# Kernel tuning notes

Measured on AMD Instinct MI355X. Metric: run time of the kernel, lower is better.

The kernel has to match this reference:

```python
import jax, jax.numpy as jnp
import numpy as np

D_IN = 1024
D_OUT = 1024
B = 4
S = 2048


def setup_inputs() -> dict:
    key = jax.random.key(0)
    kx, kq, kk, kv = jax.random.split(key, 4)
    x = jax.random.normal(kx, (B, S, D_IN), dtype=jnp.float32)
    # Linear weights stored as [d_in, d_out] so projection is x @ W
    sc = 1.0 / np.sqrt(D_IN)
    Wq = jax.random.normal(kq, (D_IN, D_OUT), dtype=jnp.float32) * sc
    Wk = jax.random.normal(kk, (D_IN, D_OUT), dtype=jnp.float32) * sc
    Wv = jax.random.normal(kv, (D_IN, D_OUT), dtype=jnp.float32) * sc
    return {"x": x, "Wq": Wq, "Wk": Wk, "Wv": Wv}


def reference(x, Wq, Wk, Wv):
    # q, k, v: [b, s, d_out]
    q = jnp.einsum("bsd,de->bse", x, Wq)
    k = jnp.einsum("bsd,de->bse", x, Wk)
    v = jnp.einsum("bsd,de->bse", x, Wv)
    s = q.shape[1]
    # raw scores [b, s, s]
    scores = jnp.einsum("bqd,bkd->bqk", q, k)
    # causal mask: disallow key j > query i (see notes re: original mask bug)
    causal = jnp.triu(jnp.ones((s, s), dtype=bool), k=1)
    scores = jnp.where(causal[None, :, :], -jnp.inf, scores)
    scale = 1.0 / jnp.sqrt(jnp.asarray(k.shape[-1], dtype=scores.dtype))
    att_weights = jax.nn.softmax(scores * scale, axis=-1)
    # dropout p=0.0 -> identity
    att_output = jnp.einsum("bqk,bkd->bqd", att_weights, v)
    return att_output, att_weights
```

## Files before the change

### kernel.cpp

```cpp
#include <hip/hip_runtime.h>
#include <stdint.h>

#define DIM 1024
#define SEQ 2048
#define NB 4

typedef unsigned short u16;
typedef __bf16 bf16x8 __attribute__((ext_vector_type(8)));
typedef float floatx4 __attribute__((ext_vector_type(4)));

__device__ __forceinline__ u16 f32_to_bf16(float f) {
  union { float f; unsigned u; } v; v.f = f;
  unsigned r = v.u + 0x7FFFu + ((v.u >> 16) & 1u);
  return (u16)(r >> 16);
}

__device__ __forceinline__ void async16(const void* g, void* l) {
  __builtin_amdgcn_global_load_lds(
      (__attribute__((address_space(1))) unsigned int*)g,
      (__attribute__((address_space(3))) unsigned int*)l, 16, 0, 0);
}

__global__ __launch_bounds__(256) void k_prep(const float* __restrict__ x,
                                              const float* __restrict__ Wq,
                                              const float* __restrict__ Wk,
                                              const float* __restrict__ Wv,
                                              u16* __restrict__ xb,
                                              u16* __restrict__ wt) {
  __shared__ u16 tile[32][33];
  const int bid = blockIdx.x;
  const int tid = threadIdx.x;
  if (bid < 4096) {
    int i = bid * 256 + tid;
    float4 a = ((const float4*)x)[i * 2];
    float4 b = ((const float4*)x)[i * 2 + 1];
    ushort4 o0, o1;
    o0.x = f32_to_bf16(a.x); o0.y = f32_to_bf16(a.y);
    o0.z = f32_to_bf16(a.z); o0.w = f32_to_bf16(a.w);
    o1.x = f32_to_bf16(b.x); o1.y = f32_to_bf16(b.y);
    o1.z = f32_to_bf16(b.z); o1.w = f32_to_bf16(b.w);
    ((ushort4*)xb)[i * 2] = o0;
    ((ushort4*)xb)[i * 2 + 1] = o1;
  } else {
    int t = bid - 4096;
    int z = t >> 10;
    int ti = t & 1023;
    int c0 = (ti & 31) * 32, r0 = (ti >> 5) * 32;
    const float* src = (z == 0) ? Wq : (z == 1) ? Wk : Wv;
    u16* d = wt + (size_t)z * DIM * DIM;
    int tx = tid & 31, ty = tid >> 5;
    #pragma unroll
    for (int dy = 0; dy < 32; dy += 8)
      tile[ty + dy][tx] = f32_to_bf16(src[(size_t)(r0 + ty + dy) * DIM + c0 + tx]);
    __syncthreads();
    #pragma unroll
    for (int dy = 0; dy < 32; dy += 8)
      d[(size_t)(c0 + ty + dy) * DIM + r0 + tx] = tile[tx][ty + dy];
  }
}


#define STG(PG, STBASE, SLOT, H, I, KT)                                        \
  async16((PG) + (size_t)((H) * 128 + (I) * 64) * DIM + (KT) * 64,             \
          (STBASE) + (SLOT) * 16384 + (H) * 8192 + (I) * 4096)

#define PHASE(SLOT, KS, MH, RDB, STGS, SYNC)                                   \
  {                                                                            \
    const int go_ = (KS) ? ga1 : ga0;                                          \
    const u16* pa_ = aRd + (SLOT) * 16384;                                     \
    if (RDB) {                                                                 \
      const u16* pb_ = bRd + (SLOT) * 16384;                                   \
      _Pragma("unroll") for (int n = 0; n < 4; ++n)                            \
          bfr[n] = *(const bf16x8*)(pb_ + n * 1024 + go_);                     \
    }                                                                          \
    _Pragma("unroll") for (int m = 0; m < 4; ++m)                              \
        af[m] = *(const bf16x8*)(pa_ + ((MH) * 4 + m) * 1024 + go_);           \
    STGS                                                                       \
    __builtin_amdgcn_s_barrier();                                              \
    asm volatile("s_waitcnt lgkmcnt(0)");                                      \
    __builtin_amdgcn_s_setprio(1);                                             \
    _Pragma("unroll") for (int m = 0; m < 4; ++m)                              \
        _Pragma("unroll") for (int n = 0; n < 4; ++n)                          \
            acc[(MH) * 4 + m][n] = __builtin_amdgcn_mfma_f32_16x16x32_bf16(    \
                af[m], bfr[n], acc[(MH) * 4 + m][n], 0, 0, 0);                 \
    __builtin_amdgcn_s_setprio(0);                                             \
    SYNC                                                                       \
    __builtin_amdgcn_s_barrier();                                              \
  }

__device__ __forceinline__ void core256(const u16* __restrict__ pga,
                                        const u16* __restrict__ pgb,
                                        const u16* aRd, const u16* bRd,
                                        u16* stA, u16* stB,
                                        int ga0, int ga1,
                                        floatx4 acc[8][4], int NITER) {
  bf16x8 af[4], bfr[4];

  STG(pga, stA, 0, 0, 0, 0); STG(pga, stA, 0, 0, 1, 0);
  STG(pga, stA, 0, 1, 0, 0); STG(pga, stA, 0, 1, 1, 0);
  STG(pgb, stB, 0, 0, 0, 0); STG(pgb, stB, 0, 0, 1, 0);
  STG(pgb, stB, 0, 1, 0, 0); STG(pgb, stB, 0, 1, 1, 0);
  STG(pgb, stB, 1, 0, 0, 1); STG(pgb, stB, 1, 0, 1, 1);
  asm volatile("s_waitcnt vmcnt(2)");
  __builtin_amdgcn_sched_barrier(0);
  __builtin_amdgcn_s_barrier();

  for (int t = 0; t < NITER; ++t) {
    const bool more = (t + 1 < NITER);
    const int kA1 = 2 * t + 1;
    const int kN = 2 * t + 2;
    const int kB1n = 2 * t + 3;

    PHASE(0, 0, 0, 1,
          { STG(pga, stA, 1, 0, 0, kA1); STG(pga, stA, 1, 0, 1, kA1); }, {})
    PHASE(0, 0, 1, 0,
          { STG(pga, stA, 1, 1, 0, kA1); STG(pga, stA, 1, 1, 1, kA1); }, {})
    PHASE(0, 1, 0, 1,
          { STG(pgb, stB, 1, 1, 0, kA1); STG(pgb, stB, 1, 1, 1, kA1); }, {})
    PHASE(0, 1, 1, 0,
          { if (more) { STG(pgb, stB, 0, 0, 0, kN); STG(pgb, stB, 0, 0, 1, kN); } },
          { if (more) { asm volatile("s_waitcnt vmcnt(2)"); }
            else      { asm volatile("s_waitcnt vmcnt(0)"); }
            __builtin_amdgcn_sched_barrier(0); })
    PHASE(1, 0, 0, 1,
          { if (more) { STG(pgb, stB, 0, 1, 0, kN); STG(pgb, stB, 0, 1, 1, kN); } }, {})
    PHASE(1, 0, 1, 0,
          { if (more) { STG(pga, stA, 0, 0, 0, kN); STG(pga, stA, 0, 0, 1, kN); } }, {})
    PHASE(1, 1, 0, 1,
          { if (more) { STG(pga, stA, 0, 1, 0, kN); STG(pga, stA, 0, 1, 1, kN); } }, {})
    PHASE(1, 1, 1, 0,
          { if (more) { STG(pgb, stB, 1, 0, 0, kB1n); STG(pgb, stB, 1, 0, 1, kB1n); } },
          { if (more) { asm volatile("s_waitcnt vmcnt(2)");
                        __builtin_amdgcn_sched_barrier(0); } })
  }

  asm volatile("s_waitcnt vmcnt(0)");
}

__global__ __launch_bounds__(512) void k_proj8(const u16* __restrict__ xb,
                                               const u16* __restrict__ wt,
                                               u16* __restrict__ qk,
                                               u16* __restrict__ vT,
                                               int base) {
  __shared__ u16 lds[65536];
  const int wg = ((blockIdx.x & 7) * 24) + (blockIdx.x >> 3) + base;
  const int tid = threadIdx.x;
  const int lane = tid & 63;
  const int wid = tid >> 6;

  const u16 *A, *Bt;
  u16* Cout;
  int ldc;
  if (wg < 256) {
    const int z = wg >> 7;
    const int r = wg & 127;
    const int mt = r >> 2, nt = r & 3;
    A = xb + (size_t)mt * 256 * DIM;
    Bt = wt + (size_t)z * DIM * DIM + (size_t)nt * 256 * DIM;
    Cout = qk + (size_t)z * (NB * SEQ * DIM) + (size_t)mt * 256 * DIM + nt * 256;
    ldc = DIM;
  } else {
    const int r = wg - 256;
    const int mt = r & 3, nt = r >> 2;
    A = wt + (size_t)2 * DIM * DIM + (size_t)mt * 256 * DIM;
    Bt = xb + (size_t)nt * 256 * DIM;
    Cout = vT + (size_t)(nt >> 3) * (DIM * SEQ) + (size_t)mt * 256 * SEQ
              + (nt & 7) * 256;
    ldc = SEQ;
  }

  const int srow = wid * 8 + (lane >> 3);
  const int gsrc = (lane & 7) ^ ((lane >> 3) & 7);
  const u16* pga = A + (size_t)srow * DIM + gsrc * 8;
  const u16* pgb = Bt + (size_t)srow * DIM + gsrc * 8;
  u16* stA = lds + wid * 512;
  u16* stB = lds + 32768 + wid * 512;

  const int wr = wid >> 2, wc = wid & 3;
  const int lrow = lane & 15, quad = lane >> 4;
  const int s = lrow & 7;
  const u16* aRd = lds + (wr * 128 + lrow) * 64;
  const u16* bRd = lds + 32768 + (wc * 64 + lrow) * 64;
  const int ga0 = (quad ^ s) << 3;
  const int ga1 = ga0 ^ 32;

  floatx4 acc[8][4] = {};
  core256(pga, pgb, aRd, bRd, stA, stB, ga0, ga1, acc, DIM / 128);

  u16* C = Cout + (size_t)(wr * 128 + quad * 4) * ldc + wc * 64 + lrow;
  #pragma unroll
  for (int m = 0; m < 8; ++m)
    #pragma unroll
    for (int rr = 0; rr < 4; ++rr)
      #pragma unroll
      for (int n = 0; n < 4; ++n)
        C[(size_t)(m * 16 + rr) * ldc + n * 16] = f32_to_bf16(acc[m][n][rr]);
}

__global__ __launch_bounds__(512) void k_scores(const u16* __restrict__ q,
                                                const u16* __restrict__ k,
                                                float* __restrict__ w) {
  __shared__ u16 lds[65536];
  const int wg = ((blockIdx.x & 7) * 32) + (blockIdx.x >> 3);
  const int tid = threadIdx.x;

  if (wg >= 144) {
    const int u = wg - 144;
    const int b = u / 28;
    int e = u % 28;
    int mt = 0, acc0 = 0;
    while (acc0 + (7 - mt) <= e) { acc0 += 7 - mt; ++mt; }
    const int nt = mt + 1 + (e - acc0);
    float4 z4 = make_float4(0.f, 0.f, 0.f, 0.f);
    const int row = tid >> 1, half = tid & 1;
    float4* p = (float4*)(w + (size_t)b * SEQ * SEQ
                            + (size_t)(mt * 256 + row) * SEQ
                            + nt * 256 + half * 128);
    #pragma unroll
    for (int kk = 0; kk < 32; ++kk) p[kk] = z4;
    return;
  }

  const int b = wg / 36;
  const int t = wg % 36;
  int mt = (int)((sqrtf(8.0f * (float)t + 1.0f) - 1.0f) * 0.5f);
  while ((mt + 1) * (mt + 2) / 2 <= t) ++mt;
  while (mt * (mt + 1) / 2 > t) --mt;
  const int nt = t - mt * (mt + 1) / 2;

  const u16* A  = q + (size_t)b * SEQ * DIM + (size_t)mt * 256 * DIM;
  const u16* Bt = k + (size_t)b * SEQ * DIM + (size_t)nt * 256 * DIM;

  const int lane = tid & 63;
  const int wid = tid >> 6;
  const int srow = wid * 8 + (lane >> 3);
  const int gsrc = (lane & 7) ^ ((lane >> 3) & 7);
  const u16* pga = A + (size_t)srow * DIM + gsrc * 8;
  const u16* pgb = Bt + (size_t)srow * DIM + gsrc * 8;
  u16* stA = lds + wid * 512;
  u16* stB = lds + 32768 + wid * 512;

  const int wr = wid >> 2, wc = wid & 3;
  const int lrow = lane & 15, quad = lane >> 4;
  const int s = lrow & 7;
  const u16* aRd = lds + (wr * 128 + lrow) * 64;
  const u16* bRd = lds + 32768 + (wc * 64 + lrow) * 64;
  const int ga0 = (quad ^ s) << 3;
  const int ga1 = ga0 ^ 32;

  floatx4 acc[8][4] = {};
  core256(pga, pgb, aRd, bRd, stA, stB, ga0, ga1, acc, DIM / 128);

  const bool diag = (mt == nt);
  const int rb = wr * 128 + quad * 4;
  const int cb = wc * 64 + lrow;
  float* C = w + (size_t)b * SEQ * SEQ
               + (size_t)(mt * 256 + rb) * SEQ + nt * 256 + cb;
  #pragma unroll
  for (int m = 0; m < 8; ++m)
    #pragma unroll
    for (int rr = 0; rr < 4; ++rr)
      #pragma unroll
      for (int n = 0; n < 4; ++n) {
        float val = acc[m][n][rr] * 0.03125f;
        if (diag && (rb + m * 16 + rr) < (cb + n * 16)) val = 0.f;
        C[(size_t)(m * 16 + rr) * SEQ + n * 16] = val;
      }
}

__device__ __forceinline__ void mfma_core128(const u16* __restrict__ A, int lda,
                                             const u16* __restrict__ Bt, int ldb,
                                             int kchunks, u16* lds,
                                             floatx4 acc[4][4]) {
  const int tid = threadIdx.x;
  const int lane = tid & 63;
  const int wid = tid >> 6;
  u16* lds_a = lds;
  u16* lds_b = lds + 16384;

  const int srow4 = lane >> 4;
  const int sgr = lane & 15;
  const int gbase = sgr ^ srow4;
  const u16* ag0 = A + (size_t)(wid * 32 + srow4) * lda + gbase * 8;
  const u16* ag1 = A + (size_t)(wid * 32 + srow4) * lda + (gbase ^ 4) * 8;
  const u16* bg0 = Bt + (size_t)(wid * 32 + srow4) * ldb + gbase * 8;
  const u16* bg1 = Bt + (size_t)(wid * 32 + srow4) * ldb + (gbase ^ 4) * 8;
  u16* la = lds_a + wid * 4096;
  u16* lb = lds_b + wid * 4096;

  const int wm = (wid >> 1) * 64, wn = (wid & 1) * 64;
  const int lrow = lane & 15, quad = lane >> 4;
  const int s = lrow & 7;
  const u16* pa = lds_a + (wm + lrow) * 128;
  const u16* pb = lds_b + (wn + lrow) * 128;

  for (int kt = 0; kt < kchunks; ++kt) {
    #pragma unroll
    for (int c = 0; c < 8; ++c) {
      const u16* sa = ((c & 1) ? ag1 : ag0) + (size_t)(c * 4) * lda;
      async16(sa, la + c * 512);
    }
    #pragma unroll
    for (int c = 0; c < 8; ++c) {
      const u16* sb = ((c & 1) ? bg1 : bg0) + (size_t)(c * 4) * ldb;
      async16(sb, lb + c * 512);
    }
    ag0 += 128; ag1 += 128; bg0 += 128; bg1 += 128;
    __syncthreads();
    #pragma unroll
    for (int ks = 0; ks < 4; ++ks) {
      const int g = (((ks << 2) | quad) ^ s) << 3;
      bf16x8 af[4], bfr[4];
      #pragma unroll
      for (int t = 0; t < 4; ++t) af[t] = *(const bf16x8*)(pa + t * 2048 + g);
      #pragma unroll
      for (int t = 0; t < 4; ++t) bfr[t] = *(const bf16x8*)(pb + t * 2048 + g);
      #pragma unroll
      for (int i = 0; i < 4; ++i)
        #pragma unroll
        for (int j = 0; j < 4; ++j)
          acc[i][j] = __builtin_amdgcn_mfma_f32_16x16x32_bf16(af[i], bfr[j],
                                                              acc[i][j], 0, 0, 0);
    }
    __syncthreads();
  }
}

__global__ __launch_bounds__(256) void k_softmax(float* __restrict__ w,
                                                 u16* __restrict__ P) {
  const int r = blockIdx.x;
  const int i = r & (SEQ - 1);
  const int len = i + 1;
  const int plen4 = (((i >> 7) + 1) << 7) >> 2;
  float4* srow = (float4*)(w + (size_t)r * SEQ);
  ushort4* prow = (ushort4*)(P + (size_t)r * SEQ);
  const int tid = threadIdx.x;
  const int lane = tid & 63, wid = tid >> 6;
  __shared__ float rm[4], rs[4];

  float4 e[2];
  float mx = -1e30f;
  #pragma unroll
  for (int u = 0; u < 2; ++u) {
    int q4 = tid + u * 256;
    int j0 = q4 * 4;
    float4 v = make_float4(-1e30f, -1e30f, -1e30f, -1e30f);
    if (j0 < len) {
      v = srow[q4];
      v.x = (j0 + 0 < len) ? v.x : -1e30f;
      v.y = (j0 + 1 < len) ? v.y : -1e30f;
      v.z = (j0 + 2 < len) ? v.z : -1e30f;
      v.w = (j0 + 3 < len) ? v.w : -1e30f;
    }
    e[u] = v;
    mx = fmaxf(mx, fmaxf(fmaxf(v.x, v.y), fmaxf(v.z, v.w)));
  }
  #pragma unroll
  for (int o = 32; o >= 1; o >>= 1) mx = fmaxf(mx, __shfl_xor(mx, o, 64));
  if (lane == 0) rm[wid] = mx;
  __syncthreads();
  mx = fmaxf(fmaxf(rm[0], rm[1]), fmaxf(rm[2], rm[3]));

  float sum = 0.f;
  #pragma unroll
  for (int u = 0; u < 2; ++u) {
    e[u].x = __expf(e[u].x - mx);
    e[u].y = __expf(e[u].y - mx);
    e[u].z = __expf(e[u].z - mx);
    e[u].w = __expf(e[u].w - mx);
    sum += e[u].x + e[u].y + e[u].z + e[u].w;
  }
  #pragma unroll
  for (int o = 32; o >= 1; o >>= 1) sum += __shfl_xor(sum, o, 64);
  if (lane == 0) rs[wid] = sum;
  __syncthreads();
  sum = rs[0] + rs[1] + rs[2] + rs[3];
  const float inv = 1.0f / sum;

  #pragma unroll
  for (int u = 0; u < 2; ++u) {
    int q4 = tid + u * 256;
    int j0 = q4 * 4;
    if (q4 < plen4) {
      float4 v;
      v.x = (j0 + 0 < len) ? e[u].x * inv : 0.f;
      v.y = (j0 + 1 < len) ? e[u].y * inv : 0.f;
      v.z = (j0 + 2 < len) ? e[u].z * inv : 0.f;
      v.w = (j0 + 3 < len) ? e[u].w * inv : 0.f;
      srow[q4] = v;
      ushort4 p;
      p.x = f32_to_bf16(v.x); p.y = f32_to_bf16(v.y);
      p.z = f32_to_bf16(v.z); p.w = f32_to_bf16(v.w);
      prow[q4] = p;
    }
  }
}

__global__ __launch_bounds__(256) void k_pv(const u16* __restrict__ P,
                                            const u16* __restrict__ vT,
                                            float* __restrict__ out) {
  const int id = blockIdx.x;
  const int mt = 15 - (id >> 5);
  const int nt = (id >> 2) & 7;
  const int b = id & 3;
  __shared__ u16 lds[32768];
  floatx4 acc[4][4] = {};
  mfma_core128(P + (size_t)b * SEQ * SEQ + (size_t)mt * 128 * SEQ, SEQ,
               vT + (size_t)b * DIM * SEQ + (size_t)nt * 128 * SEQ, SEQ,
               mt + 1, lds, acc);
  const int lane = threadIdx.x & 63, wid = threadIdx.x >> 6;
  const int wm = (wid >> 1) * 64, wn = (wid & 1) * 64;
  const int lrow = lane & 15, quad = lane >> 4;
  float* C = out + (size_t)b * SEQ * DIM
                 + (size_t)(mt * 128 + wm + quad * 4) * DIM + nt * 128 + wn + lrow;
  #pragma unroll
  for (int i = 0; i < 4; ++i)
    #pragma unroll
    for (int rr = 0; rr < 4; ++rr)
      #pragma unroll
      for (int j = 0; j < 4; ++j)
        C[(size_t)(i * 16 + rr) * DIM + j * 16] = acc[i][j][rr];
}

extern "C" void kernel_launch(void* const* d_in, const int* in_sizes, int n_in,
                              void* d_out, int out_size, void* d_ws, size_t ws_size,
                              hipStream_t stream) {
  const float* x  = (const float*)d_in[0];
  const float* Wq = (const float*)d_in[1];
  const float* Wk = (const float*)d_in[2];
  const float* Wv = (const float*)d_in[3];
  float* att_out = (float*)d_out;
  float* att_w   = (float*)d_out + 8388608;

  u16* xb = (u16*)d_ws;
  u16* wt = xb + 8388608;
  u16* qk = wt + 3145728;
  u16* vT = qk + 16777216;
  u16* P  = vT + 8388608;

  k_prep<<<7168, 256, 0, stream>>>(x, Wq, Wk, Wv, xb, wt);
  k_proj8<<<192, 512, 0, stream>>>(xb, wt, qk, vT, 0);
  k_proj8<<<192, 512, 0, stream>>>(xb, wt, qk, vT, 192);
  k_scores<<<256, 512, 0, stream>>>(qk, qk + 8388608, att_w);
  k_softmax<<<8192, 256, 0, stream>>>(att_w, P);
  k_pv<<<512, 256, 0, stream>>>(P, vT, att_out);
}
```

Before: 269.2 us.

## Merge projection launches and pair causal softmax rows per block

The two 192-block projection launches become one 384-block launch, with the block-to-tile swizzle widened to match. This removes a launch and the gap between the two kernels. The softmax kernel now handles two rows per 256-thread block, pairing row i with row 2047-i so every block does about the same causal work. Each half-block of 128 threads reduces its own row using two wavefronts. This halves the block count and evens out the triangular imbalance, at the cost of more registers per thread.

New measurement: 271.8 us. No clear change (+1.0%).

```diff
diff --git a/kernel.cpp b/kernel.cpp
--- a/kernel.cpp
+++ b/kernel.cpp
@@ -140,10 +140,9 @@
 __global__ __launch_bounds__(512) void k_proj8(const u16* __restrict__ xb,
                                                const u16* __restrict__ wt,
                                                u16* __restrict__ qk,
-                                               u16* __restrict__ vT,
-                                               int base) {
+                                               u16* __restrict__ vT) {
   __shared__ u16 lds[65536];
-  const int wg = ((blockIdx.x & 7) * 24) + (blockIdx.x >> 3) + base;
+  const int wg = ((blockIdx.x & 7) * 48) + (blockIdx.x >> 3);
   const int tid = threadIdx.x;
   const int lane = tid & 63;
   const int wid = tid >> 6;
@@ -329,20 +328,24 @@
 __global__ __launch_bounds__(256) void k_softmax(float* __restrict__ w,
                                                  u16* __restrict__ P) {
   const int r = blockIdx.x;
-  const int i = r & (SEQ - 1);
-  const int len = i + 1;
-  const int plen4 = (((i >> 7) + 1) << 7) >> 2;
-  float4* srow = (float4*)(w + (size_t)r * SEQ);
-  ushort4* prow = (ushort4*)(P + (size_t)r * SEQ);
+  const int b = r >> 10;
+  const int i = r & 1023;
   const int tid = threadIdx.x;
+  const int half = tid >> 7;
+  const int row = half ? (2047 - i) : i;
+  const int len = row + 1;
+  const int plen4 = (((row >> 7) + 1) << 7) >> 2;
+  float4* srow = (float4*)(w + ((size_t)b * SEQ + row) * SEQ);
+  ushort4* prow = (ushort4*)(P + ((size_t)b * SEQ + row) * SEQ);
+  const int t = tid & 127;
   const int lane = tid & 63, wid = tid >> 6;
   __shared__ float rm[4], rs[4];
 
-  float4 e[2];
+  float4 e[4];
   float mx = -1e30f;
   #pragma unroll
-  for (int u = 0; u < 2; ++u) {
-    int q4 = tid + u * 256;
+  for (int u = 0; u < 4; ++u) {
+    int q4 = t + u * 128;
     int j0 = q4 * 4;
     float4 v = make_float4(-1e30f, -1e30f, -1e30f, -1e30f);
     if (j0 < len) {
@@ -359,11 +362,11 @@
   for (int o = 32; o >= 1; o >>= 1) mx = fmaxf(mx, __shfl_xor(mx, o, 64));
   if (lane == 0) rm[wid] = mx;
   __syncthreads();
-  mx = fmaxf(fmaxf(rm[0], rm[1]), fmaxf(rm[2], rm[3]));
+  mx = fmaxf(rm[half * 2], rm[half * 2 + 1]);
 
   float sum = 0.f;
   #pragma unroll
-  for (int u = 0; u < 2; ++u) {
+  for (int u = 0; u < 4; ++u) {
     e[u].x = __expf(e[u].x - mx);
     e[u].y = __expf(e[u].y - mx);
     e[u].z = __expf(e[u].z - mx);
@@ -374,12 +377,12 @@
   for (int o = 32; o >= 1; o >>= 1) sum += __shfl_xor(sum, o, 64);
   if (lane == 0) rs[wid] = sum;
   __syncthreads();
-  sum = rs[0] + rs[1] + rs[2] + rs[3];
+  sum = rs[half * 2] + rs[half * 2 + 1];
   const float inv = 1.0f / sum;
 
   #pragma unroll
-  for (int u = 0; u < 2; ++u) {
-    int q4 = tid + u * 256;
+  for (int u = 0; u < 4; ++u) {
+    int q4 = t + u * 128;
     int j0 = q4 * 4;
     if (q4 < plen4) {
       float4 v;
@@ -439,9 +442,8 @@
   u16* P  = vT + 8388608;
 
   k_prep<<<7168, 256, 0, stream>>>(x, Wq, Wk, Wv, xb, wt);
-  k_proj8<<<192, 512, 0, stream>>>(xb, wt, qk, vT, 0);
-  k_proj8<<<192, 512, 0, stream>>>(xb, wt, qk, vT, 192);
+  k_proj8<<<384, 512, 0, stream>>>(xb, wt, qk, vT);
   k_scores<<<256, 512, 0, stream>>>(qk, qk + 8388608, att_w);
-  k_softmax<<<8192, 256, 0, stream>>>(att_w, P);
+  k_softmax<<<4096, 256, 0, stream>>>(att_w, P);
   k_pv<<<512, 256, 0, stream>>>(P, vT, att_out);
 }
```
